# Kernel optimization log

Hardware: AMD Instinct MI355X
Metric: run time of the kernel (lower is better)

The kernel has to match this reference:

```python
import jax, jax.numpy as jnp
import numpy as np
from jax import lax

RES = 512          # resolution
L = 16             # n_light
M = 4
N = 2 * M          # Fourier series terms
FOCAL = 50.0
CAMD = 2.7         # camera_distance
WINDOW = 1.0
SHADOW_THR = 0.008
RES_OPT = 256      # resolution_optimize
OFFSET = -0.0642233295781
CLAMP = 0.4458709375254
RBLUR = 10         # gaussian blur radius (static)

FOV = 2.0 * np.arctan(0.5 * 36.0 / FOCAL)
TANH = np.tan(FOV / 2.0)
NEAR = CAMD - np.sqrt(2.0) * CAMD * TANH
FAR = CAMD + np.sqrt(2.0) * CAMD * TANH

_rot_pi = np.array([[np.cos(np.pi), 0, np.sin(np.pi), 0], [0, 1, 0, 0],
                    [-np.sin(np.pi), 0, np.cos(np.pi), 0], [0, 0, 0, 1]], np.float32)
_m_dist = np.eye(4, dtype=np.float32); _m_dist[2, 3] = -CAMD
_local = (_rot_pi @ _m_dist).astype(np.float32)
_orth = np.array([[1.0 / WINDOW, 0, 0, 0], [0, 1.0 / WINDOW, 0, 0],
                  [0, 0, -2.0 / (FAR - NEAR), -(FAR + NEAR) / (FAR - NEAR)],
                  [0, 0, 0, 1]], np.float32)
_ck = (np.pi * (2.0 * (np.arange(M) + 1) - 1)).astype(np.float32)  # [M]


def _rotate_xyz_light(dirs):
    # dirs: [L,3] -> [L,4,4] (already transposed as in the torch permute(0,2,1))
    xd, yd, zd = dirs[:, 0], dirs[:, 1], dirs[:, 2]
    cosp = jnp.sqrt(xd * xd + zd * zd)
    cost = zd / cosp
    sint = xd / cosp
    Z = jnp.zeros_like(xd); O = jnp.ones_like(xd)
    Rn = jnp.stack([cost, -sint * yd, cosp * sint, Z,
                    Z, cosp, yd, Z,
                    -sint, -cost * yd, cosp * cost, Z,
                    Z, Z, Z, O], axis=-1).reshape(-1, 4, 4)
    return jnp.swapaxes(Rn, 1, 2)


def _blur_one(img, k):
    # img: [N,H,W], k: [2R+1]  separable gaussian, zero padding
    kh = k.reshape(1, 1, -1, 1)
    kw = k.reshape(1, 1, 1, -1)
    x = img[:, None]  # [N,1,H,W]
    x = lax.conv_general_dilated(x, kh, (1, 1), ((RBLUR, RBLUR), (0, 0)))
    x = lax.conv_general_dilated(x, kw, (1, 1), ((0, 0), (RBLUR, RBLUR)))
    return x[:, 0]


def _forward(depth, als, mask, z_map):
    res = RES
    local = jnp.asarray(_local); m_dist = jnp.asarray(_m_dist); orth = jnp.asarray(_orth)
    m1 = 2.0 * (jnp.arange(res, dtype=jnp.float32) / res + 1.0 / (2 * res)) - 1.0
    dz = depth[0, 0]                               # [res,res]
    px = -dz * TANH * m1[None, :]                  # x varies along width
    py = dz * TANH * m1[:, None]                   # y varies along height
    posw = jnp.stack([px, py, dz, jnp.ones_like(dz)], axis=-1).reshape(-1, 4)  # [V,4]
    posw_c = posw @ local.T

    mv = jnp.einsum('xy,dyz->dxz', m_dist, _rotate_xyz_light(als[:, :3]))  # [L,4,4]
    pfl = jnp.einsum('vw,dxw->dvx', posw_c, mv)
    pfl = jnp.einsum('dvw,xw->dvx', pfl, orth)      # [L,V,4]

    u = jnp.clip((res * (pfl[..., 0] + 1.0) * 0.5).astype(jnp.int32), 0, res - 1)
    v = jnp.clip((res * (pfl[..., 1] + 1.0) * 0.5).astype(jnp.int32), 0, res - 1)
    d = jnp.clip(0.5 * (1.0 + pfl[..., 2] / pfl[..., 3]), 0.0, 1.0)  # [L,V]

    li = jnp.arange(L)
    zg = z_map[li[:, None], v, u]                   # gather shadow-map depth [L,V]
    f = jnp.where(jnp.clip(d - zg, 0.0, None) > SHADOW_THR, 0.0, 1.0)

    ck = jnp.asarray(_ck)[None, :, None]            # [1,M,1]
    a_even = -2.0 * jnp.sin(ck * (d[:, None, :] + OFFSET)) / ck
    a_odd = 2.0 * jnp.cos(ck * (d[:, None, :] + OFFSET)) / ck
    a = jnp.stack([a_even, a_odd], axis=2).reshape(L, N, -1)  # interleaved [L,N,V]

    ckz = ck[..., None] * z_map[:, None]            # [L,M,res,res]
    B = jnp.stack([jnp.cos(ckz), jnp.sin(ckz)], axis=2).reshape(L, N, res, res)

    sig = (res / RES_OPT * (6.0 * als[:, 3] + 1.0) - 1.0) / 6.0   # [L]
    t = jnp.arange(-RBLUR, RBLUR + 1, dtype=jnp.float32)
    kern = jnp.exp(-0.5 * (t[None, :] / sig[:, None]) ** 2)
    kern = kern / jnp.sum(kern, axis=1, keepdims=True)            # [L,2R+1]
    D_map = jax.vmap(_blur_one)(B, kern)            # [L,N,res,res]

    ni = jnp.arange(N)
    D = D_map[li[:, None, None], ni[None, :, None], v[:, None, :], u[:, None, :]]  # [L,N,V]
    q = jnp.clip(jnp.sum(a * D, axis=1), -CLAMP, CLAMP) / CLAMP
    sf = 0.5 * (q + 1.0)

    hard = f.reshape(1, L, res, res)
    soft = jnp.clip(sf, 0.0, 1.0).reshape(1, L, res, res)
    return mask * hard, mask * soft


def setup_inputs() -> dict:
    key = jax.random.key(0)
    k1, k2, k3, k4, k5, k6 = jax.random.split(key, 6)
    depth = 2.0 + jax.random.uniform(k1, (1, 1, RES, RES), dtype=jnp.float32)
    mask = (jax.random.uniform(k2, (1, 1, RES, RES)) > 0.2).astype(jnp.float32)
    dirs = jax.random.normal(k3, (L, 3), dtype=jnp.float32)
    dirs = dirs / jnp.linalg.norm(dirs, axis=1, keepdims=True)
    sigma = 0.02 + 0.1 * jax.random.uniform(k4, (L, 1), dtype=jnp.float32)
    intensity = jax.random.uniform(k5, (L, 3), dtype=jnp.float32)
    als = jnp.concatenate([dirs, sigma, intensity], axis=1)  # [L,7]
    z_map = 0.3 + 0.7 * jax.random.uniform(k6, (L, RES, RES), dtype=jnp.float32)
    return {"depth": depth, "als": als, "mask": mask, "z_map": z_map}


def reference(depth, als, mask, z_map):
    return _forward(depth, als, mask, z_map)
```

## Files before the change

### kernel.cpp

```cpp
#include <hip/hip_runtime.h>
#include <math.h>


#define RESN 512
#define NL 16
#define NPIX (RESN*RESN)

typedef float f4a __attribute__((ext_vector_type(4), aligned(4)));

__global__ void setup_kernel(const float* __restrict__ als,
                             float* __restrict__ lp) {
  #pragma clang fp contract(off)
  int l = (int)threadIdx.x;
  if (l >= NL) return;
  float xd = als[l*7+0], yd = als[l*7+1], zd = als[l*7+2], sg = als[l*7+3];
  float cosp = sqrtf(xd*xd + zd*zd);
  float cost = zd / cosp;
  float sint = xd / cosp;
  float* o = lp + l*16;
  o[0] = cost;
  o[1] = -sint;
  o[2] = (-sint)*yd;
  o[3] = cosp;
  o[4] = (-cost)*yd;
  o[5] = cosp*sint;
  o[6] = yd;
  o[7] = cosp*cost;
  float sig = ((2.0f*(6.0f*sg + 1.0f)) - 1.0f) / 6.0f;
  float ivs = 1.0f/(sig*sig);
  float e1  = __builtin_amdgcn_exp2f(-0.72134752044448170368f*ivs);
  float e1sq = e1*e1;
  float e2  = e1sq*e1sq;
  float kinv = 1.0f/(1.0f + 2.0f*e1 + 2.0f*e2);
  float w1n = e1*kinv;
  o[8] = kinv;
  o[9] = w1n;
  o[10] = (w1n >= 0.0056f) ? 1.0f : 0.0f;
  o[11] = kinv*kinv;
  o[12] = o[13] = o[14] = o[15] = 0.0f;
}

__global__ __launch_bounds__(128) void fused_kernel(
    const float* __restrict__ depth,
    const float* __restrict__ mask,
    const float* __restrict__ z_map,
    const float* __restrict__ lp,
    float* __restrict__ out,
    float TANHF, float OZF, float OWF)
{
  #pragma clang fp contract(off)
  const float OFFS = -0.0642233295781f;
  const float CLB  = 0.4458709375254f;
  const float TWO_OVER_PI = 0.63661977236758134308f;
  const int id = (int)blockIdx.x;
  const int l0 = id >> 11;
  const int p  = ((id & 2047) << 7) + (int)threadIdx.x;
  const int r  = p >> 9, c = p & 511;

  float dz = depth[p];
  float mk = mask[p];
  float m1c = 2.0f * ((float)c / 512.0f + 0.0009765625f) - 1.0f;
  float m1r = 2.0f * ((float)r / 512.0f + 0.0009765625f) - 1.0f;
  float tT = dz * TANHF;
  float qx = tT * m1c;
  float qy = tT * m1r;
  float qz = 2.7f - dz;
  const bool live = (mk != 0.0f);

  float hard_out[2] = {0.0f, 0.0f};
  float soft_out[2] = {0.0f, 0.0f};

  if (live) {
    float rx[2], ry[2], rz[2], rw[2];
    float zT[2], zB[2];
    float wvT_[2], wvB_[2];
    float dd_[2], dpo_[2];
    float w0_[2], w1_[2], w0q_[2];
    int   u_[2], ic_[2];
    bool  ft_[2];

    #pragma unroll
    for (int k = 0; k < 2; ++k) {
      const int l = l0 + (k << 3);
      const int base = l << 18;
      const float* P = lp + l*16;
      float e00 = P[0], e02 = P[1], e10 = P[2], e11 = P[3], e12 = P[4];
      float e20 = P[5], e21 = P[6], e22 = P[7];
      w0_[k] = P[8]; w1_[k] = P[9]; w0q_[k] = P[11];
      bool ft = P[10] != 0.0f;
      ft_[k] = ft;

      float X1 = fmaf(qz, e02, qx * e00);
      float Y1 = fmaf(qz, e12, fmaf(qy, e11, qx * e10));
      float T2 = fmaf(qz, e22, fmaf(qy, e21, qx * e20));
      float Z1 = T2 + (-2.7f);
      float ZZ = (Z1 * OZF) + OWF;
      float uf = (X1 + 1.0f) * 256.0f;
      float vf = (Y1 + 1.0f) * 256.0f;
      int u = (int)uf; u = u < 0 ? 0 : (u > 511 ? 511 : u);
      int v = (int)vf; v = v < 0 ? 0 : (v > 511 ? 511 : v);
      float dd = 0.5f * (1.0f + ZZ);
      dd = fminf(fmaxf(dd, 0.0f), 1.0f);
      dd_[k] = dd; dpo_[k] = dd + OFFS;
      u_[k] = u;

      const float* zrC = z_map + base + (v << 9);
      if (ft) {
        int b = (u - 1) & ~1;
        b = b < 0 ? 0 : (b > 508 ? 508 : b);
        f4a rv = *reinterpret_cast<const f4a*>(zrC + b);
        rx[k] = rv.x; ry[k] = rv.y; rz[k] = rv.z; rw[k] = rv.w;
        ic_[k] = u - b;
        int v0 = v > 0 ? v - 1 : 0;
        int v2 = v < 511 ? v + 1 : 511;
        zT[k] = z_map[base + (v0 << 9) + u];
        zB[k] = z_map[base + (v2 << 9) + u];
        wvT_[k] = (v > 0)   ? w1_[k] : 0.0f;
        wvB_[k] = (v < 511) ? w1_[k] : 0.0f;
      } else {
        ry[k] = zrC[u];
        ic_[k] = 1;
        wvT_[k] = wvB_[k] = 0.0f;
      }
    }

    __builtin_amdgcn_sched_barrier(0x7);

    #pragma unroll
    for (int k = 0; k < 2; ++k) {
      const float dpo = dpo_[k];
      auto fval = [&](float z) {
        float s = __builtin_amdgcn_sinf(0.5f * (z - dpo));
        float t = s * s;
        return s * fmaf(t, fmaf(t, fmaf(t, -9.142857142857142f, 19.2f),
                                -13.333333333333334f), 4.0f);
      };
      float w0 = w0_[k], w1 = w1_[k];
      float q, zg;
      if (ft_[k]) {
        bool e0 = ic_[k] == 0, e2 = ic_[k] == 2, e3 = ic_[k] == 3;
        float zC = e0 ? rx[k] : e2 ? rz[k] : e3 ? rw[k] : ry[k];
        float zL = e0 ? rx[k] : e2 ? ry[k] : e3 ? rz[k] : rx[k];
        float zR = e0 ? ry[k] : (e2 | e3) ? rw[k] : rz[k];
        int u = u_[k];
        float wuL = (u > 0)   ? w1 : 0.0f;
        float wuR = (u < 511) ? w1 : 0.0f;
        float qs = w0 * fval(zC);
        qs = fmaf(wvT_[k], fval(zT[k]), qs);
        qs = fmaf(wvB_[k], fval(zB[k]), qs);
        qs = fmaf(wuL, fval(zL), qs);
        qs = fmaf(wuR, fval(zR), qs);
        q = TWO_OVER_PI * (w0 * qs);
        zg = zC;
      } else {
        zg = ry[k];
        q = TWO_OVER_PI * (w0q_[k] * fval(zg));
      }
      float diff = fmaxf(dd_[k] - zg, 0.0f);
      hard_out[k] = mk * ((diff > 0.008f) ? 0.0f : 1.0f);
      float qc = fminf(fmaxf(q, -CLB), CLB) / CLB;
      float sf = 0.5f * (qc + 1.0f);
      soft_out[k] = mk * fminf(fmaxf(sf, 0.0f), 1.0f);
    }
  }

  #pragma unroll
  for (int k = 0; k < 2; ++k) {
    const int base = (l0 + (k << 3)) << 18;
    out[base + p] = hard_out[k];
    out[(NL*NPIX) + base + p] = soft_out[k];
  }
}

extern "C" void kernel_launch(void* const* d_in, const int* in_sizes, int n_in,
                              void* d_out, int out_size, void* d_ws, size_t ws_size,
                              hipStream_t stream) {
  (void)in_sizes; (void)n_in; (void)out_size; (void)ws_size;
  const float* depth = (const float*)d_in[0];
  const float* als   = (const float*)d_in[1];
  const float* mask  = (const float*)d_in[2];
  const float* z_map = (const float*)d_in[3];
  float* out = (float*)d_out;
  float* lp = (float*)d_ws;
  double TANH = tan(2.0*atan(0.5*36.0/50.0)/2.0);
  double NEARc = 2.7 - sqrt(2.0)*2.7*TANH;
  double FARc  = 2.7 + sqrt(2.0)*2.7*TANH;
  float ozf = (float)(-2.0/(FARc-NEARc));
  float owf = (float)((-(FARc+NEARc))/(FARc-NEARc));
  float tanhf_ = (float)TANH;

  setup_kernel<<<1, 64, 0, stream>>>(als, lp);
  fused_kernel<<<(NL/2)*NPIX/128, 128, 0, stream>>>(depth, mask, z_map, lp,
                                                    out, tanhf_, ozf, owf);
}
```

Measured before the change: 102.1 us.

## Pre-transpose z_map so vertical neighbour taps load as one vector

Adds a tiled shared-memory transpose kernel that writes a column-major copy of z_map for every light whose blur filter is active. The main kernel then fetches the up and down neighbours with one aligned 4-float load from the transposed copy instead of two scattered scalar loads. This adds a full extra read and write pass over z_map (up to 16 MB each way) plus a third kernel launch, traded against fewer random gathers in the fused kernel.

```diff
diff --git a/kernel.cpp b/kernel.cpp
--- a/kernel.cpp
+++ b/kernel.cpp
@@ -40,10 +40,39 @@
   o[12] = o[13] = o[14] = o[15] = 0.0f;
 }
 
+__global__ __launch_bounds__(256) void transpose_kernel(
+    const float* __restrict__ z_map,
+    const float* __restrict__ lp,
+    float* __restrict__ zt) {
+  const int bid = (int)blockIdx.x;
+  const int l = bid >> 8;
+  if (lp[l*16 + 10] == 0.0f) return;
+  const int tile = bid & 255;
+  const int u0 = (tile & 15) << 5;
+  const int v0 = (tile >> 4) << 5;
+  __shared__ float t[32][33];
+  const int tx = (int)threadIdx.x & 31;
+  const int ty = (int)threadIdx.x >> 5;
+  const float* src = z_map + (l << 18);
+  float* dst = zt + (l << 18);
+  #pragma unroll
+  for (int i = 0; i < 4; ++i) {
+    int v = v0 + ty + (i << 3);
+    t[ty + (i << 3)][tx] = src[(v << 9) + u0 + tx];
+  }
+  __syncthreads();
+  #pragma unroll
+  for (int i = 0; i < 4; ++i) {
+    int u = u0 + ty + (i << 3);
+    dst[(u << 9) + v0 + tx] = t[tx][ty + (i << 3)];
+  }
+}
+
 __global__ __launch_bounds__(128) void fused_kernel(
     const float* __restrict__ depth,
     const float* __restrict__ mask,
     const float* __restrict__ z_map,
+    const float* __restrict__ zt,
     const float* __restrict__ lp,
     float* __restrict__ out,
     float TANHF, float OZF, float OWF)
@@ -72,11 +101,11 @@
 
   if (live) {
     float rx[2], ry[2], rz[2], rw[2];
-    float zT[2], zB[2];
+    float tx_[2], ty_[2], tz_[2], tw_[2];
     float wvT_[2], wvB_[2];
     float dd_[2], dpo_[2];
     float w0_[2], w1_[2], w0q_[2];
-    int   u_[2], ic_[2];
+    int   u_[2], ic_[2], ic2_[2];
     bool  ft_[2];
 
     #pragma unroll
@@ -111,15 +140,17 @@
         f4a rv = *reinterpret_cast<const f4a*>(zrC + b);
         rx[k] = rv.x; ry[k] = rv.y; rz[k] = rv.z; rw[k] = rv.w;
         ic_[k] = u - b;
-        int v0 = v > 0 ? v - 1 : 0;
-        int v2 = v < 511 ? v + 1 : 511;
-        zT[k] = z_map[base + (v0 << 9) + u];
-        zB[k] = z_map[base + (v2 << 9) + u];
+        int b2 = (v - 1) & ~1;
+        b2 = b2 < 0 ? 0 : (b2 > 508 ? 508 : b2);
+        f4a tv = *reinterpret_cast<const f4a*>(zt + base + (u << 9) + b2);
+        tx_[k] = tv.x; ty_[k] = tv.y; tz_[k] = tv.z; tw_[k] = tv.w;
+        ic2_[k] = v - b2;
         wvT_[k] = (v > 0)   ? w1_[k] : 0.0f;
         wvB_[k] = (v < 511) ? w1_[k] : 0.0f;
       } else {
         ry[k] = zrC[u];
         ic_[k] = 1;
+        ic2_[k] = 1;
         wvT_[k] = wvB_[k] = 0.0f;
       }
     }
@@ -142,12 +173,15 @@
         float zC = e0 ? rx[k] : e2 ? rz[k] : e3 ? rw[k] : ry[k];
         float zL = e0 ? rx[k] : e2 ? ry[k] : e3 ? rz[k] : rx[k];
         float zR = e0 ? ry[k] : (e2 | e3) ? rw[k] : rz[k];
+        int i2 = ic2_[k];
+        float zT = (i2 >= 2) ? ((i2 == 2) ? ty_[k] : tz_[k]) : tx_[k];
+        float zB = (i2 == 0) ? ty_[k] : ((i2 == 1) ? tz_[k] : tw_[k]);
         int u = u_[k];
         float wuL = (u > 0)   ? w1 : 0.0f;
         float wuR = (u < 511) ? w1 : 0.0f;
         float qs = w0 * fval(zC);
-        qs = fmaf(wvT_[k], fval(zT[k]), qs);
-        qs = fmaf(wvB_[k], fval(zB[k]), qs);
+        qs = fmaf(wvT_[k], fval(zT), qs);
+        qs = fmaf(wvB_[k], fval(zB), qs);
         qs = fmaf(wuL, fval(zL), qs);
         qs = fmaf(wuR, fval(zR), qs);
         q = TWO_OVER_PI * (w0 * qs);
@@ -182,6 +216,7 @@
   const float* z_map = (const float*)d_in[3];
   float* out = (float*)d_out;
   float* lp = (float*)d_ws;
+  float* zt = (float*)((char*)d_ws + 4096);
   double TANH = tan(2.0*atan(0.5*36.0/50.0)/2.0);
   double NEARc = 2.7 - sqrt(2.0)*2.7*TANH;
   double FARc  = 2.7 + sqrt(2.0)*2.7*TANH;
@@ -190,6 +225,7 @@
   float tanhf_ = (float)TANH;
 
   setup_kernel<<<1, 64, 0, stream>>>(als, lp);
-  fused_kernel<<<(NL/2)*NPIX/128, 128, 0, stream>>>(depth, mask, z_map, lp,
+  transpose_kernel<<<NL*256, 256, 0, stream>>>(z_map, lp, zt);
+  fused_kernel<<<(NL/2)*NPIX/128, 128, 0, stream>>>(depth, mask, z_map, zt, lp,
                                                     out, tanhf_, ozf, owf);
 }
```

Result: slower. 106.4 us (+4.2%).
